# Kernel tuning notes

Hardware: AMD Instinct MI355X
Metric: run time of the kernel (lower is better)

The kernel has to match this reference:

```python
import jax, jax.numpy as jnp
import numpy as np

H = 16            # num_heads
SEG = 2048        # segment_size
DIL = 8           # dilation_rate
BLOCK_M = 64      # triton query block size (min(64, M_padded))


def setup_inputs() -> dict:
    key = jax.random.key(0)
    k1, k2, k3 = jax.random.split(key, 3)
    B, M, D = 2, 8192, 1024
    x = jax.random.normal(k1, (B, M, D), dtype=jnp.float32)
    Wqkv = jax.random.normal(k2, (3 * D, D), dtype=jnp.float32) * 0.02
    Wout = jax.random.normal(k3, (D, D), dtype=jnp.float32) * 0.02
    return {"x": x, "Wqkv": Wqkv, "Wout": Wout}


def reference(x, Wqkv, Wout):
    B, M, D = x.shape
    hd = D // H
    scale = hd ** -0.5
    S = M // SEG                      # number of segments (M is a multiple of SEG)
    Kn = SEG // DIL                   # dilated keys per segment
    nb = SEG // BLOCK_M               # query blocks per segment

    # qkv projection (torch Linear: x @ W^T), split into q,k,v: [B,H,M,hd]
    qkv = jnp.einsum('bmd,ed->bme', x, Wqkv).reshape(B, M, 3, H, hd)
    qkv = jnp.transpose(qkv, (2, 0, 3, 1, 4))
    q, k, v = qkv[0] * scale, qkv[1], qkv[2]

    # segment-local views
    q4 = q.reshape(B, H, S, SEG, hd)
    k4 = k.reshape(B, H, S, SEG, hd)[:, :, :, ::DIL]   # [B,H,S,Kn,hd] dilated keys
    v4 = v.reshape(B, H, S, SEG, hd)[:, :, :, ::DIL]

    # scores per segment: [B,H,S,SEG,Kn]
    scores = jnp.einsum('bhspd,bhskd->bhspk', q4, k4)
    # kernel normalization: per key j, subtract max over the 64-query block
    scores = scores.reshape(B, H, S, nb, BLOCK_M, Kn)
    c = jnp.max(scores, axis=4, keepdims=True)          # [B,H,S,nb,1,Kn]
    w = jnp.exp(scores - c)
    den = jnp.sum(w, axis=-1) + 1e-10                   # [B,H,S,nb,BLOCK_M]
    num = jnp.einsum('bhsnmk,bhskd->bhsnmd', w, v4)
    out = num / den[..., None]                          # [B,H,S,nb,BLOCK_M,hd]

    out = out.reshape(B, H, M, hd)
    out = jnp.transpose(out, (0, 2, 1, 3)).reshape(B, M, D)
    return jnp.einsum('bmd,ed->bme', out, Wout)
```

## Files before the change

### kernel.cpp

```cpp
#include <hip/hip_runtime.h>
#include <hip/hip_bf16.h>
#include <stdint.h>


typedef __attribute__((ext_vector_type(8))) short short8;
typedef __attribute__((ext_vector_type(4))) float f32x4;

#define DEVI static __device__ __forceinline__

DEVI unsigned short f2bf(float f) {
  union { float f; uint32_t u; } v; v.f = f;
  return (unsigned short)((v.u + 0x7FFFu + ((v.u >> 16) & 1u)) >> 16);
}

DEVI uint32_t pack_bf16(float lo, float hi) {
  return (uint32_t)f2bf(lo) | ((uint32_t)f2bf(hi) << 16);
}

DEVI uint32_t pack_hu(float lo, float hi) {
  union { float f; uint32_t u; } a, b; a.f = lo; b.f = hi;
  return ((a.u + 0x8000u) >> 16) | ((b.u + 0x8000u) & 0xFFFF0000u);
}

DEVI void gload_lds16(const void* g, void* l) {
  __builtin_amdgcn_global_load_lds((const __attribute__((address_space(1))) void*)g,
                                   (__attribute__((address_space(3))) void*)l,
                                   16, 0, 0);
}

__global__ void cvt_kernel(const float* __restrict__ in, unsigned short* __restrict__ out, int n) {
  int i = (blockIdx.x * 256 + threadIdx.x) * 4;
  if (i >= n) return;
  float4 f = *(const float4*)(in + i);
  uint2 o;
  o.x = (uint32_t)f2bf(f.x) | ((uint32_t)f2bf(f.y) << 16);
  o.y = (uint32_t)f2bf(f.z) | ((uint32_t)f2bf(f.w) << 16);
  *(uint2*)(out + i) = o;
}

#define STAGE_A(bf, hf, kt) do { \
  gload_lds16(Abase + (long)((hf) * 128 + srow0) * 1024 + (kt) * 64 + scol0, &smA[bf][hf][se0]); \
  gload_lds16(Abase + (long)((hf) * 128 + srow1) * 1024 + (kt) * 64 + scol1, &smA[bf][hf][se1]); \
} while (0)
#define STAGE_B(bf, hf, kt) do { \
  gload_lds16(Bbase + (long)((hf) * 128 + srow0) * 1024 + (kt) * 64 + scol0, &smB[bf][hf][se0]); \
  gload_lds16(Bbase + (long)((hf) * 128 + srow1) * 1024 + (kt) * 64 + scol1, &smB[bf][hf][se1]); \
} while (0)

template<bool OUT_F32>
__global__ __launch_bounds__(512, 1) void gemm8p(
    const unsigned short* __restrict__ A, const unsigned short* __restrict__ B,
    void* __restrict__ Cv, float scale)
{
  __shared__ unsigned short smA[2][2][128 * 64];
  __shared__ unsigned short smB[2][2][128 * 64];
  const int tid = threadIdx.x;
  const int tm = blockIdx.x, tn = blockIdx.y;
  const int w = tid >> 6, lane = tid & 63;
  const int wm = w >> 2, wn = w & 3;
  const int lr = lane & 15, lq = lane >> 4;

  const int e0 = tid * 8,        e1 = (512 + tid) * 8;
  const int srow0 = e0 >> 6,     srow1 = e1 >> 6;
  const int sc0 = (e0 >> 3) & 7, sc1 = (e1 >> 3) & 7;
  const int scol0 = (sc0 ^ (srow0 & 7)) * 8, scol1 = (sc1 ^ (srow1 & 7)) * 8;
  const int se0 = e0, se1 = e1;

  const unsigned short* Abase = A + (long)tm * 256 * 1024;
  const unsigned short* Bbase = B + (long)tn * 256 * 1024;

  f32x4 acc[8][4] = {};
  short8 af[4][2];
  short8 bfr[2][2][2];

  STAGE_A(0, 0, 0); STAGE_B(0, 0, 0); STAGE_B(0, 1, 0); STAGE_A(0, 1, 0);
  asm volatile("s_waitcnt vmcnt(4)" ::: "memory");
  __builtin_amdgcn_s_barrier();
  asm volatile("" ::: "memory");

  for (int t = 0; t < 8; ++t) {
#pragma unroll
    for (int p = 0; p < 8; ++p) {
      const int o = p >> 2;
      const int q = p & 3;
      const int a = (p >> 1) & 1;
      const int b = a ^ (q & 1);

      if (q == 0 || q == 2) {
#pragma unroll
        for (int mi2 = 0; mi2 < 4; ++mi2) {
          int r = wm * 64 + mi2 * 16 + lr;
#pragma unroll
          for (int kk = 0; kk < 2; ++kk) {
            int kc = kk * 4 + lq;
            af[mi2][kk] = *(const short8*)&smA[o][a][r * 64 + ((kc ^ (r & 7)) * 8)];
          }
        }
      }
      if (q == 0 || q == 1) {
#pragma unroll
        for (int nj2 = 0; nj2 < 2; ++nj2) {
          int r = wn * 32 + nj2 * 16 + lr;
#pragma unroll
          for (int kk = 0; kk < 2; ++kk) {
            int kc = kk * 4 + lq;
            bfr[b][nj2][kk] = *(const short8*)&smB[o][b][r * 64 + ((kc ^ (r & 7)) * 8)];
          }
        }
      }

      switch (p) {
        case 0: STAGE_A(1, 0, 2 * t + 1); STAGE_B(1, 0, 2 * t + 1); break;
        case 2: STAGE_B(1, 1, 2 * t + 1); STAGE_A(1, 1, 2 * t + 1); break;
        case 4: if (t < 7) { STAGE_A(0, 0, 2 * t + 2); STAGE_B(0, 0, 2 * t + 2); } break;
        case 6: if (t < 7) { STAGE_B(0, 1, 2 * t + 2); STAGE_A(0, 1, 2 * t + 2); } break;
      }

      __builtin_amdgcn_s_barrier();
      if (q != 3) {
        asm volatile("s_waitcnt lgkmcnt(0)" ::: "memory");
        __builtin_amdgcn_sched_barrier(0);
      }

      __builtin_amdgcn_s_setprio(1);
#pragma unroll
      for (int kk = 0; kk < 2; ++kk)
#pragma unroll
        for (int mi2 = 0; mi2 < 4; ++mi2)
#pragma unroll
          for (int nj2 = 0; nj2 < 2; ++nj2)
            acc[a * 4 + mi2][b * 2 + nj2] = __builtin_amdgcn_mfma_f32_16x16x32_bf16(
                af[mi2][kk], bfr[b][nj2][kk], acc[a * 4 + mi2][b * 2 + nj2], 0, 0, 0);
      __builtin_amdgcn_s_setprio(0);

      if (t < 7) {
        if (p == 0 || p == 3 || p == 4 || p == 7)
          asm volatile("s_waitcnt vmcnt(4)" ::: "memory");
      } else {
        if (p == 0 || p == 3)  asm volatile("s_waitcnt vmcnt(4)" ::: "memory");
        else if (p == 4)       asm volatile("s_waitcnt vmcnt(0)" ::: "memory");
      }
      __builtin_amdgcn_s_barrier();
      asm volatile("" ::: "memory");
    }
  }

  const int row0 = tm * 256 + wm * 64 + lq * 4;
  const int col0 = tn * 256 + wn * 32 + lr;
#pragma unroll
  for (int mi = 0; mi < 8; ++mi) {
    int row = row0 + (mi & 3) * 16 + (mi >> 2) * 128;
#pragma unroll
    for (int nj = 0; nj < 4; ++nj) {
      int col = col0 + (nj & 1) * 16 + (nj >> 1) * 128;
#pragma unroll
      for (int rr = 0; rr < 4; ++rr) {
        float v = acc[mi][nj][rr] * scale;
        long off = (long)(row + rr) * 1024 + col;
        if (OUT_F32) ((float*)Cv)[off] = v;
        else         ((unsigned short*)Cv)[off] = f2bf(v);
      }
    }
  }
}

template<int EPI>
__global__ __launch_bounds__(256, 2) void gemm_bt(
    const unsigned short* __restrict__ A, const unsigned short* __restrict__ B,
    void* __restrict__ Cv, unsigned short* __restrict__ Cv2,
    float scale, long a_row_stride, int ldc, int K)
{
  __shared__ unsigned short smA[128 * 64];
  __shared__ unsigned short smB[128 * 64];
  const int tid = threadIdx.x;
  const int tm = blockIdx.x, tn = blockIdx.y;
  const int w = tid >> 6, lane = tid & 63;
  const int wr = (w >> 1) * 64, wc = (w & 1) * 64;
  const int lr = lane & 15, lq = lane >> 4;

  int se[4], srow[4], scol[4];
#pragma unroll
  for (int i = 0; i < 4; ++i) {
    int e = (i * 256 + tid) * 8;
    int r = e >> 6;
    int cc = (e >> 3) & 7;
    se[i] = e; srow[i] = r; scol[i] = (cc ^ (r & 7)) * 8;
  }

  f32x4 acc[4][4] = {};

  for (int kt = 0; kt < K / 64; ++kt) {
    if (kt) __syncthreads();
#pragma unroll
    for (int i = 0; i < 4; ++i)
      gload_lds16(A + (long)(tm * 128 + srow[i]) * a_row_stride + kt * 64 + scol[i], &smA[se[i]]);
#pragma unroll
    for (int i = 0; i < 4; ++i)
      gload_lds16(B + (long)(tn * 128 + srow[i]) * K + kt * 64 + scol[i], &smB[se[i]]);
    __syncthreads();

#pragma unroll
    for (int kk = 0; kk < 2; ++kk) {
      int kc = kk * 4 + lq;
      short8 af[4], bfm[4];
#pragma unroll
      for (int i = 0; i < 4; ++i) {
        int row = wr + i * 16 + lr;
        af[i] = *(const short8*)&smA[row * 64 + ((kc ^ (row & 7)) * 8)];
      }
#pragma unroll
      for (int j = 0; j < 4; ++j) {
        int row = wc + j * 16 + lr;
        bfm[j] = *(const short8*)&smB[row * 64 + ((kc ^ (row & 7)) * 8)];
      }
#pragma unroll
      for (int i = 0; i < 4; ++i)
#pragma unroll
        for (int j = 0; j < 4; ++j)
          acc[i][j] = __builtin_amdgcn_mfma_f32_16x16x32_bf16(af[i], bfm[j], acc[i][j], 0, 0, 0);
    }
  }

  if (EPI == 2 && tn >= 8) {
    const int fbase = (tn - 8) * 128 + wc;
#pragma unroll
    for (int ip = 0; ip < 4; ip += 2) {
      int t0 = tm * 128 + wr + ip * 16 + lq * 4;
      int seg = t0 >> 8;
      int ts  = t0 & 255;
      int c32 = (ts >> 5) * 16 + (ts & 15);
#pragma unroll
      for (int j = 0; j < 4; ++j) {
        int f = fbase + j * 16 + lr;
        uint32_t* rp = (uint32_t*)&Cv2[((long)(seg * 1024 + f)) * 256];
        uint4 U;
        U.x = pack_bf16(acc[ip][j][0] * scale, acc[ip + 1][j][0] * scale);
        U.y = pack_bf16(acc[ip][j][1] * scale, acc[ip + 1][j][1] * scale);
        U.z = pack_bf16(acc[ip][j][2] * scale, acc[ip + 1][j][2] * scale);
        U.w = pack_bf16(acc[ip][j][3] * scale, acc[ip + 1][j][3] * scale);
        *(uint4*)&rp[c32] = U;
      }
    }
    return;
  }

#pragma unroll
  for (int i = 0; i < 4; ++i) {
    int rg0 = tm * 128 + wr + i * 16 + lq * 4;
#pragma unroll
    for (int j = 0; j < 4; ++j) {
      int cg = tn * 128 + wc + j * 16 + lr;
#pragma unroll
      for (int r = 0; r < 4; ++r) {
        float v = acc[i][j][r] * scale;
        long off = (long)(rg0 + r) * ldc + cg;
        if (EPI == 0) ((float*)Cv)[off] = v;
        else          ((unsigned short*)Cv)[off] = f2bf(v);
      }
    }
  }
}

__global__ __launch_bounds__(512, 2) void attn_kernel(
    const unsigned short* __restrict__ qb,
    const unsigned short* __restrict__ kb,
    const unsigned short* __restrict__ vtb,
    unsigned short* __restrict__ attout)
{
  __shared__ uint32_t w32[8][64][20];

  const int u = (blockIdx.x & 7) * 64 + (blockIdx.x >> 3);
  const int quarter = u & 3, h = (u >> 2) & 15, s = (u >> 6) & 3, b = u >> 8;
  const int tid = threadIdx.x, w = tid >> 6, lane = tid & 63;
  const int lr = lane & 15, lq = lane >> 4;
  const long qrow0 = (long)b * 8192 + s * 2048 + quarter * 512 + w * 64;
  const int hc = h * 64;

  const unsigned short* kbase = kb + ((long)(b * 4 + s) * 256) * 1024 + hc;
  const unsigned short* vbase = vtb + ((long)(b * 4 + s) * 1024 + hc) * 256;

  const unsigned short* qbase = qb + qrow0 * 1024 + hc;
  short8 aq[4][2];
#pragma unroll
  for (int i = 0; i < 4; ++i)
#pragma unroll
    for (int kk = 0; kk < 2; ++kk)
      aq[i][kk] = *(const short8*)&qbase[(i * 16 + lr) * 1024 + (kk * 4 + lq) * 8];

  short8 ones;
#pragma unroll
  for (int e = 0; e < 8; ++e) ones[e] = (short)0x3F80;

  uint32_t (*wsl)[20] = w32[w];

  f32x4 acc_pv[4][4] = {};
  f32x4 acc_den[4] = {};
  short8 bk0[2][2], bk1[2][2];
  f32x4 sA[4][2], sB[4][2];

#define LOADK(BK, CC) do { \
  _Pragma("unroll") for (int j = 0; j < 2; ++j) \
    _Pragma("unroll") for (int kk = 0; kk < 2; ++kk) \
      BK[j][kk] = *(const short8*)&kbase[(long)((CC) * 32 + j * 16 + lr) * 1024 + (kk * 4 + lq) * 8]; \
} while (0)

#define QKT(S, BK) do { \
  _Pragma("unroll") for (int i = 0; i < 4; ++i) \
    _Pragma("unroll") for (int j = 0; j < 2; ++j) { \
      f32x4 z = {0.f, 0.f, 0.f, 0.f}; S[i][j] = z; } \
  _Pragma("unroll") for (int kk = 0; kk < 2; ++kk) \
    _Pragma("unroll") for (int i = 0; i < 4; ++i) \
      _Pragma("unroll") for (int j = 0; j < 2; ++j) \
        S[i][j] = __builtin_amdgcn_mfma_f32_16x16x32_bf16(aq[i][kk], BK[j][kk], S[i][j], 0, 0, 0); \
} while (0)

#define SOFTPV(S, CC) do { \
   \
  short8 av_[4]; \
  _Pragma("unroll") for (int ct = 0; ct < 4; ++ct) \
    av_[ct] = *(const short8*)&vbase[(ct * 16 + lr) * 256 + ((CC) * 4 + lq) * 8]; \
   \
  float p0[4], p1[4]; \
  _Pragma("unroll") for (int i = 0; i < 4; ++i) { \
    p0[i] = fmaxf(fmaxf(S[i][0][0], S[i][0][1]), fmaxf(S[i][0][2], S[i][0][3])); \
    p1[i] = fmaxf(fmaxf(S[i][1][0], S[i][1][1]), fmaxf(S[i][1][2], S[i][1][3])); \
  } \
  float c0 = fmaxf(fmaxf(p0[0], p0[1]), fmaxf(p0[2], p0[3])); \
  float c1 = fmaxf(fmaxf(p1[0], p1[1]), fmaxf(p1[2], p1[3])); \
  c0 = fmaxf(c0, __shfl_xor(c0, 16)); c0 = fmaxf(c0, __shfl_xor(c0, 32)); \
  c1 = fmaxf(c1, __shfl_xor(c1, 16)); c1 = fmaxf(c1, __shfl_xor(c1, 32)); \
  _Pragma("unroll") for (int i = 0; i < 4; ++i) \
    _Pragma("unroll") for (int r = 0; r < 4; ++r) { \
      int qq = i * 16 + lq * 4 + r; \
      wsl[qq][lr] = pack_hu(__expf(S[i][0][r] - c0), __expf(S[i][1][r] - c1)); } \
  _Pragma("unroll") for (int qi = 0; qi < 4; ++qi) { \
    short8 bw = *(const short8*)&wsl[qi * 16 + lr][lq * 4]; \
    acc_den[qi] = __builtin_amdgcn_mfma_f32_16x16x32_bf16(ones, bw, acc_den[qi], 0, 0, 0); \
    _Pragma("unroll") for (int ct = 0; ct < 4; ++ct) \
      acc_pv[qi][ct] = __builtin_amdgcn_mfma_f32_16x16x32_bf16(av_[ct], bw, acc_pv[qi][ct], 0, 0, 0); } \
} while (0)

  LOADK(bk0, 0);
  LOADK(bk1, 1);
  QKT(sA, bk0);

  LOADK(bk0, 2); QKT(sB, bk1); SOFTPV(sA, 0);
  LOADK(bk1, 3); QKT(sA, bk0); SOFTPV(sB, 1);
  LOADK(bk0, 4); QKT(sB, bk1); SOFTPV(sA, 2);
  LOADK(bk1, 5); QKT(sA, bk0); SOFTPV(sB, 3);
  LOADK(bk0, 6); QKT(sB, bk1); SOFTPV(sA, 4);
  LOADK(bk1, 7); QKT(sA, bk0); SOFTPV(sB, 5);
                 QKT(sB, bk1); SOFTPV(sA, 6);
                               SOFTPV(sB, 7);

#pragma unroll
  for (int qi = 0; qi < 4; ++qi) {
    float inv = 1.0f / (acc_den[qi][0] + 1e-10f);
    long orow = (qrow0 + qi * 16 + lr) * 1024 + hc;
#pragma unroll
    for (int ct = 0; ct < 4; ++ct) {
      uint2 p;
      p.x = pack_hu(acc_pv[qi][ct][0] * inv, acc_pv[qi][ct][1] * inv);
      p.y = pack_hu(acc_pv[qi][ct][2] * inv, acc_pv[qi][ct][3] * inv);
      *(uint2*)&attout[orow + ct * 16 + lq * 4] = p;
    }
  }
}

extern "C" void kernel_launch(void* const* d_in, const int* in_sizes, int n_in,
                              void* d_out, int out_size, void* d_ws, size_t ws_size,
                              hipStream_t stream) {
  (void)in_sizes; (void)n_in; (void)out_size; (void)ws_size;
  const float* x    = (const float*)d_in[0];
  const float* Wqkv = (const float*)d_in[1];
  const float* Wout = (const float*)d_in[2];
  float* out = (float*)d_out;
  char* ws = (char*)d_ws;

  unsigned short* xb     = (unsigned short*)(ws);
  unsigned short* attout = (unsigned short*)(ws);
  unsigned short* wqkvb  = (unsigned short*)(ws + 33554432);
  unsigned short* woutb  = (unsigned short*)(ws + 39845888);
  unsigned short* qbuf   = (unsigned short*)(ws + 41943040);
  unsigned short* kbuf   = (unsigned short*)(ws + 75497472);
  unsigned short* vtb    = (unsigned short*)(ws + 79691776);

  cvt_kernel<<<16384, 256, 0, stream>>>(x, xb, 16777216);
  cvt_kernel<<<3072, 256, 0, stream>>>(Wqkv, wqkvb, 3 * 1024 * 1024);
  cvt_kernel<<<1024, 256, 0, stream>>>(Wout, woutb, 1024 * 1024);

  gemm8p<false><<<dim3(64, 4), 512, 0, stream>>>(xb, wqkvb, (void*)qbuf, 0.125f);
  gemm_bt<2><<<dim3(16, 16), 256, 0, stream>>>(
      xb, wqkvb + 1024 * 1024, (void*)kbuf, vtb, 1.0f, 8192, 1024, 1024);

  attn_kernel<<<512, 512, 0, stream>>>(qbuf, kbuf, vtb, attout);

  gemm8p<true><<<dim3(64, 4), 512, 0, stream>>>(attout, woutb, (void*)out, 1.0f);
}
```

Measured before the change: 170.1 us.

## Stage V tile in swizzled LDS and coalesce fp32 GEMM epilogue via scratch

The attention kernel now copies the whole per-segment transposed V slice (64x256 bf16) into LDS once per block with an XOR swizzle. It then reads the V fragments from LDS instead of issuing scattered global loads in every softmax/PV step. Separately, the fp32 output path of the large GEMM stages each accumulator tile through padded LDS scratch so it can write float4 rows instead of scalar strided stores. The extra LDS use (32KB) may reduce occupancy, and the epilogue adds LDS round-trips and waits.

Measured after the change: 167.9 us. Within noise of the previous version (-1.3%).

```diff
diff --git a/kernel.cpp b/kernel.cpp
--- a/kernel.cpp
+++ b/kernel.cpp
@@ -145,20 +145,46 @@
     }
   }
 
-  const int row0 = tm * 256 + wm * 64 + lq * 4;
-  const int col0 = tn * 256 + wn * 32 + lr;
-#pragma unroll
-  for (int mi = 0; mi < 8; ++mi) {
-    int row = row0 + (mi & 3) * 16 + (mi >> 2) * 128;
-#pragma unroll
-    for (int nj = 0; nj < 4; ++nj) {
-      int col = col0 + (nj & 1) * 16 + (nj >> 1) * 128;
-#pragma unroll
-      for (int rr = 0; rr < 4; ++rr) {
-        float v = acc[mi][nj][rr] * scale;
-        long off = (long)(row + rr) * 1024 + col;
-        if (OUT_F32) ((float*)Cv)[off] = v;
-        else         ((unsigned short*)Cv)[off] = f2bf(v);
+  if (OUT_F32) {
+    float* scratch = (float*)&smA[0][0][0] + w * 544;
+    float* Cf = (float*)Cv;
+#pragma unroll
+    for (int ai = 0; ai < 8; ++ai) {
+#pragma unroll
+      for (int b2 = 0; b2 < 2; ++b2) {
+#pragma unroll
+        for (int nj2 = 0; nj2 < 2; ++nj2)
+#pragma unroll
+          for (int rr = 0; rr < 4; ++rr)
+            scratch[(lq * 4 + rr) * 33 + nj2 * 16 + lr] = acc[ai][b2 * 2 + nj2][rr] * scale;
+        asm volatile("s_waitcnt lgkmcnt(0)" ::: "memory");
+        __builtin_amdgcn_sched_barrier(0);
+        int rr2 = lane >> 2, cb = (lane & 3) * 8;
+        float4 v0, v1;
+        v0.x = scratch[rr2 * 33 + cb + 0]; v0.y = scratch[rr2 * 33 + cb + 1];
+        v0.z = scratch[rr2 * 33 + cb + 2]; v0.w = scratch[rr2 * 33 + cb + 3];
+        v1.x = scratch[rr2 * 33 + cb + 4]; v1.y = scratch[rr2 * 33 + cb + 5];
+        v1.z = scratch[rr2 * 33 + cb + 6]; v1.w = scratch[rr2 * 33 + cb + 7];
+        asm volatile("s_waitcnt lgkmcnt(0)" ::: "memory");
+        __builtin_amdgcn_sched_barrier(0);
+        long rowg = tm * 256 + wm * 64 + (ai & 3) * 16 + (ai >> 2) * 128 + rr2;
+        long colg = tn * 256 + wn * 32 + b2 * 128 + cb;
+        *(float4*)&Cf[rowg * 1024 + colg] = v0;
+        *(float4*)&Cf[rowg * 1024 + colg + 4] = v1;
+      }
+    }
+  } else {
+    const int row0 = tm * 256 + wm * 64 + lq * 4;
+    const int col0 = tn * 256 + wn * 32 + lr;
+#pragma unroll
+    for (int mi = 0; mi < 8; ++mi) {
+      int row = row0 + (mi & 3) * 16 + (mi >> 2) * 128;
+#pragma unroll
+      for (int nj = 0; nj < 4; ++nj) {
+        int col = col0 + (nj & 1) * 16 + (nj >> 1) * 128;
+#pragma unroll
+        for (int rr = 0; rr < 4; ++rr)
+          ((unsigned short*)Cv)[(long)(row + rr) * 1024 + col] = f2bf(acc[mi][nj][rr] * scale);
       }
     }
   }
@@ -267,6 +293,7 @@
     const unsigned short* __restrict__ vtb,
     unsigned short* __restrict__ attout)
 {
+  __shared__ unsigned short v_t[64 * 256];
   __shared__ uint32_t w32[8][64][20];
 
   const int u = (blockIdx.x & 7) * 64 + (blockIdx.x >> 3);
@@ -279,6 +306,14 @@
   const unsigned short* kbase = kb + ((long)(b * 4 + s) * 256) * 1024 + hc;
   const unsigned short* vbase = vtb + ((long)(b * 4 + s) * 1024 + hc) * 256;
 
+#pragma unroll
+  for (int it = 0; it < 4; ++it) {
+    int e = (it * 512 + tid) * 8;
+    int f = e >> 8;
+    int ch = (e >> 3) & 31;
+    gload_lds16(vbase + (long)f * 256 + ((ch ^ (f & 7)) * 8), &v_t[e]);
+  }
+
   const unsigned short* qbase = qb + qrow0 * 1024 + hc;
   short8 aq[4][2];
 #pragma unroll
@@ -286,6 +321,8 @@
 #pragma unroll
     for (int kk = 0; kk < 2; ++kk)
       aq[i][kk] = *(const short8*)&qbase[(i * 16 + lr) * 1024 + (kk * 4 + lq) * 8];
+
+  __syncthreads();
 
   short8 ones;
 #pragma unroll
@@ -315,10 +352,6 @@
 } while (0)
 
 #define SOFTPV(S, CC) do { \
-   \
-  short8 av_[4]; \
-  _Pragma("unroll") for (int ct = 0; ct < 4; ++ct) \
-    av_[ct] = *(const short8*)&vbase[(ct * 16 + lr) * 256 + ((CC) * 4 + lq) * 8]; \
    \
   float p0[4], p1[4]; \
   _Pragma("unroll") for (int i = 0; i < 4; ++i) { \
@@ -333,6 +366,10 @@
     _Pragma("unroll") for (int r = 0; r < 4; ++r) { \
       int qq = i * 16 + lq * 4 + r; \
       wsl[qq][lr] = pack_hu(__expf(S[i][0][r] - c0), __expf(S[i][1][r] - c1)); } \
+  short8 av_[4]; \
+  _Pragma("unroll") for (int ct = 0; ct < 4; ++ct) { \
+    int frow = ct * 16 + lr; \
+    av_[ct] = *(const short8*)&v_t[frow * 256 + ((((CC) * 4 + lq) ^ (frow & 7)) << 3)]; } \
   _Pragma("unroll") for (int qi = 0; qi < 4; ++qi) { \
     short8 bw = *(const short8*)&wsl[qi * 16 + lr][lq * 4]; \
     acc_den[qi] = __builtin_amdgcn_mfma_f32_16x16x32_bf16(ones, bw, acc_den[qi], 0, 0, 0); \
```
